# Kernel optimization log

Measured on AMD Instinct MI355X. Metric: run time of the kernel, lower is better.

Reference implementation:

```python
import jax, jax.numpy as jnp
import numpy as np

CONTEXT = 3  # matches init_kwargs

def _shift_fwd(x, d):
    # out[:, d:, :] = x[:, :-d, :] ; zeros in front
    N = x.shape[1]
    return jnp.pad(x, ((0, 0), (d, 0), (0, 0)))[:, :N, :]

def _shift_bwd(x, d):
    # out[:, :-d, :] = x[:, d:, :] ; zeros at end
    return jnp.pad(x, ((0, 0), (0, d), (0, 0)))[:, d:, :]

def _pairing(x_l, x_r, context):
    if context <= 1:
        return x_l, x_r
    # NB: torch source initializes both lists with x_l (faithful reproduction)
    z_l, z_r = [x_l], [x_l]
    for d in range(1, context // 2 + 1):
        z_l.append(_shift_fwd(x_l, d))   # z_lu
        z_r.append(_shift_bwd(x_r, d))   # z_ru
        z_l.append(_shift_bwd(x_l, d))   # z_ld
        z_r.append(_shift_fwd(x_r, d))   # z_rd
    return jnp.concatenate(z_l, axis=2), jnp.concatenate(z_r, axis=2)

def setup_inputs() -> dict:
    key = jax.random.key(0)
    ks = jax.random.split(key, 8)
    B, N, n_in = 2, 512, 64
    n = n_in * CONTEXT  # 192
    H = 128
    n_out = 8
    s = 0.05
    return {
        "x_l": jax.random.normal(ks[0], (B, N, n_in), jnp.float32),
        "x_r": jax.random.normal(ks[1], (B, N, n_in), jnp.float32),
        "fc_l_W": jax.random.normal(ks[2], (H, n), jnp.float32) * s,
        "fc_l_b": jax.random.normal(ks[3], (H,), jnp.float32) * s,
        "fc_r_W": jax.random.normal(ks[4], (H, n), jnp.float32) * s,
        "fc_r_b": jax.random.normal(ks[5], (H,), jnp.float32) * s,
        "bilinear_W": jax.random.normal(ks[6], (n_out, H, H), jnp.float32) * s,
        "bilinear_b": jax.random.normal(ks[7], (n_out,), jnp.float32) * s,
    }

def reference(x_l, x_r, fc_l_W, fc_l_b, fc_r_W, fc_r_b, bilinear_W, bilinear_b):
    # context-shift pairing: [B,N,n_in] -> [B,N,n_in*context]
    zl, zr = _pairing(x_l, x_r, CONTEXT)
    # per-position MLP with CELU (dropout_rate=0 -> identity)
    hl = jax.nn.celu(jnp.einsum('bnf,hf->bnh', zl, fc_l_W) + fc_l_b)
    hr = jax.nn.celu(jnp.einsum('bnf,hf->bnh', zr, fc_r_W) + fc_r_b)
    # bilinear over the NxN pair grid without materializing [B,N,N,H]:
    # out[b,i,j,o] = hl[b,i] @ W[o] @ hr[b,j] + b[o]
    t = jnp.einsum('bih,ohg->biog', hl, bilinear_W)   # [B,N,n_out,H]
    out = jnp.einsum('biog,bjg->bijo', t, hr) + bilinear_b
    return out  # [B,N,N,n_out]
```

## Files before the change

### kernel.cpp

```cpp
#include <hip/hip_runtime.h>
#include <math.h>

#define BB 2
#define NN 512
#define NIN 64
#define NF 192
#define HH 128
#define NOUT 8

typedef short short8 __attribute__((ext_vector_type(8)));
typedef float f32x4 __attribute__((ext_vector_type(4)));

__device__ __forceinline__ float celu1(float x) {
    return x > 0.0f ? x : expm1f(x);
}

__device__ __forceinline__ ushort f2b(float f) {
    union { float f; uint u; } v; v.f = f;
    uint r = v.u + 0x7fffu + ((v.u >> 16) & 1u);
    return (ushort)(r >> 16);
}
__device__ __forceinline__ uint pack2(float a, float b) {
    return (uint)f2b(a) | ((uint)f2b(b) << 16);
}
__device__ __forceinline__ short8 cvt8(const float* __restrict__ p) {
    float4 a = *(const float4*)p;
    float4 b = *(const float4*)(p + 4);
    union { uint4 u; short8 s; } c;
    c.u.x = pack2(a.x, a.y); c.u.y = pack2(a.z, a.w);
    c.u.z = pack2(b.x, b.y); c.u.w = pack2(b.z, b.w);
    return c.s;
}

__global__ __launch_bounds__(256) void k1_kernel(
    const float* __restrict__ x_l, const float* __restrict__ x_r,
    const float* __restrict__ Wl, const float* __restrict__ bl,
    const float* __restrict__ Wr, const float* __restrict__ br,
    const float* __restrict__ Wb,
    ushort* __restrict__ hl_bf, ushort* __restrict__ hr_bf,
    ushort* __restrict__ Wt)
{
    __shared__ float lds[128 * 65];
    int blk = blockIdx.x;
    int tid = threadIdx.x;

    if (blk < 256) {
        int mb = blk & 63;
        int lr = (blk >> 6) & 1;
        int hh = blk >> 7;
        int m0 = mb * 16;
        int b  = m0 >> 9;
        int i_base = m0 & (NN - 1);

        int wave = tid >> 6;
        int lane = tid & 63;
        int lrow = lane & 15;
        int lgrp = lane >> 4;
        int h0 = hh * 64 + wave * 16;
        int i = i_base + lrow;

        const float* Wm   = lr ? Wr : Wl;
        const float* bias = lr ? br : bl;
        const float* xa   = lr ? x_r : x_l;
        ushort* dst       = lr ? hr_bf : hl_bf;

        short8 bf[6];
        #pragma unroll
        for (int kk = 0; kk < 6; ++kk) {
            int part = kk >> 1;
            int c0 = (kk & 1) * 32 + lgrp * 8;
            int s; const float* src;
            if (part == 0)      { s = 0;            src = x_l; }
            else if (part == 1) { s = lr ? +1 : -1; src = xa; }
            else                { s = lr ? -1 : +1; src = xa; }
            int row = i + s;
            short8 v = (short8)0;
            if ((unsigned)row < (unsigned)NN)
                v = cvt8(&src[(b * NN + row) * NIN + c0]);
            bf[kk] = v;
        }

        f32x4 acc = (f32x4)(0.0f);
        #pragma unroll
        for (int kk = 0; kk < 6; ++kk) {
            short8 afrag = cvt8(&Wm[(h0 + lrow) * NF + kk * 32 + lgrp * 8]);
            acc = __builtin_amdgcn_mfma_f32_16x16x32_bf16(afrag, bf[kk], acc, 0, 0, 0);
        }

        int h_base = h0 + lgrp * 4;
        float4 bv = *(const float4*)&bias[h_base];
        int m = m0 + lrow;
        uint2 v;
        v.x = pack2(celu1(acc[0] + bv.x), celu1(acc[1] + bv.y));
        v.y = pack2(celu1(acc[2] + bv.z), celu1(acc[3] + bv.w));
        *(uint2*)&dst[m * HH + h_base] = v;
    } else {
        int o = blk - 256;
        for (int h0 = 0; h0 < HH; h0 += 64) {
            for (int idx = tid; idx < 64 * 128; idx += 256) {
                int hh = idx >> 7;
                int g  = idx & 127;
                lds[g * 65 + hh] = Wb[(o * HH + h0 + hh) * HH + g];
            }
            __syncthreads();
            for (int idx = tid; idx < 128 * 64; idx += 256) {
                int g  = idx >> 6;
                int hh = idx & 63;
                Wt[(o * HH + g) * HH + h0 + hh] = f2b(lds[g * 65 + hh]);
            }
            __syncthreads();
        }
    }
}

#define TSTR 136

__global__ __launch_bounds__(1024) void k2_kernel(
    const ushort* __restrict__ hl_bf, const ushort* __restrict__ hr_bf,
    const ushort* __restrict__ Wt, const float* __restrict__ bias,
    float* __restrict__ out)
{
    __shared__ ushort t_s[128 * TSTR];

    int j0 = blockIdx.x * 128;
    int i0 = blockIdx.y * 16;
    int b  = blockIdx.z;
    int tid  = threadIdx.x;
    int wave = tid >> 6;
    int lane = tid & 63;
    int lrow = lane & 15;
    int lgrp = lane >> 4;

    int jt = wave & 7;
    int jw = j0 + jt * 16;
    const ushort* hb = hr_bf + (size_t)b * NN * HH;
    short8 bfr[4];
    #pragma unroll
    for (int kk = 0; kk < 4; ++kk)
        bfr[kk] = *(const short8*)&hb[(jw + lrow) * HH + kk * 32 + lgrp * 8];

    short8 hfrag[4];
    #pragma unroll
    for (int kk = 0; kk < 4; ++kk)
        hfrag[kk] = *(const short8*)&hl_bf[(b * NN + i0 + lrow) * HH + kk * 32 + lgrp * 8];

    int o_p1 = wave >> 1;
    int gh   = wave & 1;
    #pragma unroll
    for (int gt = 0; gt < 4; ++gt) {
        int g_base = gh * 64 + gt * 16;
        f32x4 acc = (f32x4)(0.0f);
        #pragma unroll
        for (int kk = 0; kk < 4; ++kk) {
            short8 afrag = *(const short8*)&Wt[(o_p1 * HH + g_base + lrow) * HH + kk * 32 + lgrp * 8];
            acc = __builtin_amdgcn_mfma_f32_16x16x32_bf16(afrag, hfrag[kk], acc, 0, 0, 0);
        }
        int row = o_p1 * 16 + lrow;
        int gg = g_base + lgrp * 4;
        uint2 v;
        v.x = pack2(acc[0], acc[1]);
        v.y = pack2(acc[2], acc[3]);
        *(uint2*)&t_s[row * TSTR + gg] = v;
    }
    __syncthreads();

    int og = (wave >> 3) * 4;
    f32x4 acc2[4];
    #pragma unroll
    for (int s = 0; s < 4; ++s) acc2[s] = (f32x4)(0.0f);

    #pragma unroll
    for (int kk = 0; kk < 4; ++kk) {
        int koff = kk * 32 + lgrp * 8;
        #pragma unroll
        for (int s = 0; s < 4; ++s) {
            short8 afr = *(const short8*)&t_s[((og + s) * 16 + lrow) * TSTR + koff];
            acc2[s] = __builtin_amdgcn_mfma_f32_16x16x32_bf16(afr, bfr[kk], acc2[s], 0, 0, 0);
        }
    }

    int j = jw + lrow;
    #pragma unroll
    for (int s = 0; s < 4; ++s) {
        int o = og + s;
        float bv = bias[o];
        #pragma unroll
        for (int r = 0; r < 4; ++r) {
            int i = i0 + lgrp * 4 + r;
            out[((size_t)((b * NN + i) * NN + j)) * NOUT + o] = acc2[s][r] + bv;
        }
    }
}

extern "C" void kernel_launch(void* const* d_in, const int* in_sizes, int n_in,
                              void* d_out, int out_size, void* d_ws, size_t ws_size,
                              hipStream_t stream) {
    const float* x_l  = (const float*)d_in[0];
    const float* x_r  = (const float*)d_in[1];
    const float* Wl   = (const float*)d_in[2];
    const float* bl   = (const float*)d_in[3];
    const float* Wr   = (const float*)d_in[4];
    const float* br   = (const float*)d_in[5];
    const float* Wb   = (const float*)d_in[6];
    const float* bb   = (const float*)d_in[7];
    float* out = (float*)d_out;

    ushort* hl_bf = (ushort*)d_ws;
    ushort* hr_bf = hl_bf + BB * NN * HH;
    ushort* Wt    = hr_bf + BB * NN * HH;

    k1_kernel<<<264, 256, 0, stream>>>(x_l, x_r, Wl, bl, Wr, br, Wb,
                                       hl_bf, hr_bf, Wt);
    k2_kernel<<<dim3(NN / 128, NN / 16, BB), 1024, 0, stream>>>(
        hl_bf, hr_bf, Wt, bb, out);
}
```

Before: 33.24 us.

## Reorder t rows as (i,o) so bilinear output stores become float4

The intermediate t tile is stored in shared memory with rows indexed by i*8+o instead of o*16+i, using an XOR swizzle in place of padding to avoid bank conflicts. Each wave's accumulator then holds four consecutive output channels for one (i,j), so results go out as float4 stores instead of scattered scalar stores. The block shrinks from 1024 to 512 threads, and each wave now computes all eight m-subtiles, which doubles per-wave MFMA work and accumulator registers.

```diff
diff --git a/kernel.cpp b/kernel.cpp
--- a/kernel.cpp
+++ b/kernel.cpp
@@ -113,14 +113,18 @@
     }
 }
 
-#define TSTR 136
-
-__global__ __launch_bounds__(1024) void k2_kernel(
+__device__ __forceinline__ ushort* tsw(ushort* t_s, int m, int col) {
+    int key = (m ^ (m >> 3)) & 7;
+    int byte = m * 256 + ((col * 2) ^ (key << 4));
+    return (ushort*)((char*)t_s + byte);
+}
+
+__global__ __launch_bounds__(512) void k2_kernel(
     const ushort* __restrict__ hl_bf, const ushort* __restrict__ hr_bf,
     const ushort* __restrict__ Wt, const float* __restrict__ bias,
     float* __restrict__ out)
 {
-    __shared__ ushort t_s[128 * TSTR];
+    __shared__ ushort t_s[128 * 128];
 
     int j0 = blockIdx.x * 128;
     int i0 = blockIdx.y * 16;
@@ -131,8 +135,7 @@
     int lrow = lane & 15;
     int lgrp = lane >> 4;
 
-    int jt = wave & 7;
-    int jw = j0 + jt * 16;
+    int jw = j0 + wave * 16;
     const ushort* hb = hr_bf + (size_t)b * NN * HH;
     short8 bfr[4];
     #pragma unroll
@@ -144,51 +147,56 @@
     for (int kk = 0; kk < 4; ++kk)
         hfrag[kk] = *(const short8*)&hl_bf[(b * NN + i0 + lrow) * HH + kk * 32 + lgrp * 8];
 
-    int o_p1 = wave >> 1;
-    int gh   = wave & 1;
-    #pragma unroll
-    for (int gt = 0; gt < 4; ++gt) {
-        int g_base = gh * 64 + gt * 16;
+    int o_p1 = wave;
+    #pragma unroll
+    for (int gt = 0; gt < 8; ++gt) {
+        int g_base = gt * 16;
         f32x4 acc = (f32x4)(0.0f);
         #pragma unroll
         for (int kk = 0; kk < 4; ++kk) {
             short8 afrag = *(const short8*)&Wt[(o_p1 * HH + g_base + lrow) * HH + kk * 32 + lgrp * 8];
             acc = __builtin_amdgcn_mfma_f32_16x16x32_bf16(afrag, hfrag[kk], acc, 0, 0, 0);
         }
-        int row = o_p1 * 16 + lrow;
+        int m  = lrow * 8 + o_p1;
         int gg = g_base + lgrp * 4;
         uint2 v;
         v.x = pack2(acc[0], acc[1]);
         v.y = pack2(acc[2], acc[3]);
-        *(uint2*)&t_s[row * TSTR + gg] = v;
+        *(uint2*)tsw(t_s, m, gg) = v;
     }
     __syncthreads();
 
-    int og = (wave >> 3) * 4;
-    f32x4 acc2[4];
-    #pragma unroll
-    for (int s = 0; s < 4; ++s) acc2[s] = (f32x4)(0.0f);
+    f32x4 acc2[8];
+    #pragma unroll
+    for (int ms = 0; ms < 8; ++ms) acc2[ms] = (f32x4)(0.0f);
 
     #pragma unroll
     for (int kk = 0; kk < 4; ++kk) {
         int koff = kk * 32 + lgrp * 8;
         #pragma unroll
-        for (int s = 0; s < 4; ++s) {
-            short8 afr = *(const short8*)&t_s[((og + s) * 16 + lrow) * TSTR + koff];
-            acc2[s] = __builtin_amdgcn_mfma_f32_16x16x32_bf16(afr, bfr[kk], acc2[s], 0, 0, 0);
-        }
-    }
-
+        for (int ms = 0; ms < 8; ++ms) {
+            short8 afr = *(const short8*)tsw(t_s, ms * 16 + lrow, koff);
+            acc2[ms] = __builtin_amdgcn_mfma_f32_16x16x32_bf16(afr, bfr[kk], acc2[ms], 0, 0, 0);
+        }
+    }
+
+    float4 b0 = *(const float4*)&bias[0];
+    float4 b1 = *(const float4*)&bias[4];
     int j = jw + lrow;
-    #pragma unroll
-    for (int s = 0; s < 4; ++s) {
-        int o = og + s;
-        float bv = bias[o];
-        #pragma unroll
-        for (int r = 0; r < 4; ++r) {
-            int i = i0 + lgrp * 4 + r;
-            out[((size_t)((b * NN + i) * NN + j)) * NOUT + o] = acc2[s][r] + bv;
-        }
+
+    #pragma unroll
+    for (int ms = 0; ms < 8; ++ms) {
+        int m_base = ms * 16 + lgrp * 4;
+        int i  = i0 + (m_base >> 3);
+        int o0 = m_base & 7;
+        float4 bv = o0 ? b1 : b0;
+        float4 v;
+        v.x = acc2[ms][0] + bv.x;
+        v.y = acc2[ms][1] + bv.y;
+        v.z = acc2[ms][2] + bv.z;
+        v.w = acc2[ms][3] + bv.w;
+        float* dst = out + ((size_t)((b * NN + i) * NN + j)) * NOUT + o0;
+        *(float4*)dst = v;
     }
 }
 
@@ -211,6 +219,6 @@
 
     k1_kernel<<<264, 256, 0, stream>>>(x_l, x_r, Wl, bl, Wr, br, Wb,
                                        hl_bf, hr_bf, Wt);
-    k2_kernel<<<dim3(NN / 128, NN / 16, BB), 1024, 0, stream>>>(
+    k2_kernel<<<dim3(NN / 128, NN / 16, BB), 512, 0, stream>>>(
         hl_bf, hr_bf, Wt, bb, out);
 }
```

New measurement: 27.15 us. 18.3% less time.
